# Kernel tuning notes

Measured on AMD Instinct MI355X. Metric: run time of the kernel, lower is better.

## Reference

```python
import jax, jax.numpy as jnp
import numpy as np


def setup_inputs() -> dict:
    key = jax.random.key(0)
    k1, k2 = jax.random.split(key)
    emb_in = jax.random.normal(k1, (2048, 32), dtype=jnp.float32)
    sum_weights = jax.random.normal(k2, (2048,), dtype=jnp.float32)
    return {"emb_in": emb_in, "sum_weights": sum_weights}


def reference(emb_in, sum_weights):
    # emb_in: [n, f], sum_weights: [n]
    n, f = emb_in.shape
    # a[k] = emb_in[k // n]  (each row repeated n times consecutively)
    a = jnp.repeat(emb_in, n, axis=0)          # [n*n, f]
    # b[k] = emb_in[k % n]   (whole tensor tiled n times)
    b = jnp.tile(emb_in, (n, 1))               # [n*n, f]
    # weights column matches b: w[k] = sum_weights[k % n]
    w = jnp.tile(sum_weights[:, None], (n, 1)) # [n*n, 1]
    sample = jnp.concatenate((a, b, w), axis=1)  # [n*n, 2*f + 1]
    return sample
```

## Files before the change

kernel.cpp:

```cpp
#include <hip/hip_runtime.h>


#define NROWS 2048u
#define BLOCK_ROWS 512u
#define WAVE_ROWS 128u
#define SLAB_ROWS 16u
#define NSLABS 8u
#define SLAB_FLOATS (SLAB_ROWS * 65u)
#define SLAB_F4 (SLAB_FLOATS / 4u)

typedef float f32x4 __attribute__((ext_vector_type(4)));

__global__ __launch_bounds__(256) void expand_pipe(
    const float* __restrict__ emb,
    const float* __restrict__ sw,
    f32x4* __restrict__ out)
{
    __shared__ __align__(16) float lds[4][2][SLAB_FLOATS];

    const unsigned tid  = threadIdx.x;
    const unsigned wave = tid >> 6;
    const unsigned lane = tid & 63u;

    const unsigned r0 = blockIdx.x * BLOCK_ROWS + wave * WAVE_ROWS;
    const unsigned i  = r0 >> 11;
    const unsigned j0 = r0 & (NROWS - 1u);

    const float vi = emb[i * 32u + (lane & 31u)];
    const unsigned rbase = (lane >> 5) * 8u;
#pragma unroll
    for (unsigned b = 0; b < 2u; ++b)
#pragma unroll
        for (unsigned rp = 0; rp < 8u; ++rp)
            lds[wave][b][(rbase + rp) * 65u + (lane & 31u)] = vi;

    const unsigned d0 = (lane >> 3) * 65u + 32u + (lane & 7u) * 4u;

    {
        const f32x4* ej = (const f32x4*)(emb + (size_t)j0 * 32u);
        const f32x4 pa = ej[lane];
        const f32x4 pb = ej[lane + 64u];
        const float ps = sw[j0 + (lane & 15u)];
        float* B = &lds[wave][0][0];
        B[d0 + 0u] = pa.x; B[d0 + 1u] = pa.y;
        B[d0 + 2u] = pa.z; B[d0 + 3u] = pa.w;
        B[d0 + 520u + 0u] = pb.x; B[d0 + 520u + 1u] = pb.y;
        B[d0 + 520u + 2u] = pb.z; B[d0 + 520u + 3u] = pb.w;
        if (lane < 16u) B[lane * 65u + 64u] = ps;
    }

#pragma unroll
    for (unsigned s = 0; s < NSLABS; ++s) {
        const unsigned cur = s & 1u;

        f32x4 pa, pb;
        float ps = 0.0f;
        if (s + 1u < NSLABS) {
            const f32x4* ej =
                (const f32x4*)(emb + (size_t)(j0 + (s + 1u) * SLAB_ROWS) * 32u);
            pa = ej[lane];
            pb = ej[lane + 64u];
            ps = sw[j0 + (s + 1u) * SLAB_ROWS + (lane & 15u)];
        }

        const f32x4* L4 = (const f32x4*)&lds[wave][cur][0];
        const unsigned obase = ((r0 + s * SLAB_ROWS) >> 4) * SLAB_F4;
#pragma unroll
        for (unsigned p = 0; p < 4u; ++p)
            out[obase + p * 64u + lane] = L4[p * 64u + lane];
        if (lane < 4u)
            out[obase + 256u + lane] = L4[256u + lane];

        if (s + 1u < NSLABS) {
            float* B = &lds[wave][cur ^ 1u][0];
            B[d0 + 0u] = pa.x; B[d0 + 1u] = pa.y;
            B[d0 + 2u] = pa.z; B[d0 + 3u] = pa.w;
            B[d0 + 520u + 0u] = pb.x; B[d0 + 520u + 1u] = pb.y;
            B[d0 + 520u + 2u] = pb.z; B[d0 + 520u + 3u] = pb.w;
            if (lane < 16u) B[lane * 65u + 64u] = ps;
        }
    }
}

extern "C" void kernel_launch(void* const* d_in, const int* in_sizes, int n_in,
                              void* d_out, int out_size, void* d_ws, size_t ws_size,
                              hipStream_t stream) {
    const float* emb = (const float*)d_in[0];
    const float* sw  = (const float*)d_in[1];
    f32x4* out       = (f32x4*)d_out;

    const unsigned blocks = (NROWS * NROWS) / BLOCK_ROWS;
    expand_pipe<<<dim3(blocks), dim3(256), 0, stream>>>(emb, sw, out);
}
```

Measured before the change: 203.9 us.

## Replace LDS double buffer with register double buffering and two-slab prefetch

Drops the per-wave second LDS buffer and instead reads each assembled slab from LDS into registers, alternating between two register sets. Global loads for the next slabs are issued two slabs ahead, and the LDS slot is rewritten right after being read, so stores to the output come straight from registers. The aim is to halve LDS use and hide global load latency behind the output stores, at the cost of higher VGPR pressure. The kernel is store-bound, so the gain may be small.

```diff
diff --git a/kernel.cpp b/kernel.cpp
--- a/kernel.cpp
+++ b/kernel.cpp
@@ -11,12 +11,12 @@
 
 typedef float f32x4 __attribute__((ext_vector_type(4)));
 
-__global__ __launch_bounds__(256) void expand_pipe(
+__global__ __launch_bounds__(256) void expand_rra(
     const float* __restrict__ emb,
     const float* __restrict__ sw,
     f32x4* __restrict__ out)
 {
-    __shared__ __align__(16) float lds[4][2][SLAB_FLOATS];
+    __shared__ __align__(16) float lds[4][SLAB_FLOATS];
 
     const unsigned tid  = threadIdx.x;
     const unsigned wave = tid >> 6;
@@ -26,60 +26,84 @@
     const unsigned i  = r0 >> 11;
     const unsigned j0 = r0 & (NROWS - 1u);
 
+    float* W = &lds[wave][0];
+    const f32x4* L4 = (const f32x4*)W;
+
     const float vi = emb[i * 32u + (lane & 31u)];
     const unsigned rbase = (lane >> 5) * 8u;
 #pragma unroll
-    for (unsigned b = 0; b < 2u; ++b)
-#pragma unroll
-        for (unsigned rp = 0; rp < 8u; ++rp)
-            lds[wave][b][(rbase + rp) * 65u + (lane & 31u)] = vi;
+    for (unsigned rp = 0; rp < 8u; ++rp)
+        W[(rbase + rp) * 65u + (lane & 31u)] = vi;
 
     const unsigned d0 = (lane >> 3) * 65u + 32u + (lane & 7u) * 4u;
 
+    f32x4 RA0, RA1, RA2, RA3, RA4;
+    f32x4 RB0, RB1, RB2, RB3, RB4;
+    f32x4 pA0, pA1, pB0, pB1;
+    float psA, psB;
+
     {
         const f32x4* ej = (const f32x4*)(emb + (size_t)j0 * 32u);
-        const f32x4 pa = ej[lane];
-        const f32x4 pb = ej[lane + 64u];
-        const float ps = sw[j0 + (lane & 15u)];
-        float* B = &lds[wave][0][0];
-        B[d0 + 0u] = pa.x; B[d0 + 1u] = pa.y;
-        B[d0 + 2u] = pa.z; B[d0 + 3u] = pa.w;
-        B[d0 + 520u + 0u] = pb.x; B[d0 + 520u + 1u] = pb.y;
-        B[d0 + 520u + 2u] = pb.z; B[d0 + 520u + 3u] = pb.w;
-        if (lane < 16u) B[lane * 65u + 64u] = ps;
+        const f32x4 a0 = ej[lane];
+        const f32x4 a1 = ej[lane + 64u];
+        const float s0 = sw[j0 + (lane & 15u)];
+        W[d0 + 0u] = a0.x; W[d0 + 1u] = a0.y;
+        W[d0 + 2u] = a0.z; W[d0 + 3u] = a0.w;
+        W[d0 + 520u] = a1.x; W[d0 + 521u] = a1.y;
+        W[d0 + 522u] = a1.z; W[d0 + 523u] = a1.w;
+        if (lane < 16u) W[lane * 65u + 64u] = s0;
+    }
+    {
+        const f32x4* ej = (const f32x4*)(emb + (size_t)(j0 + SLAB_ROWS) * 32u);
+        pB0 = ej[lane];
+        pB1 = ej[lane + 64u];
+        psB = sw[j0 + SLAB_ROWS + (lane & 15u)];
+    }
+    RA0 = L4[lane];         RA1 = L4[64u + lane];
+    RA2 = L4[128u + lane];  RA3 = L4[192u + lane];
+    RA4 = L4[256u + (lane & 3u)];
+
+    const unsigned base0 = (r0 >> 4) * SLAB_F4;
+
+#define STEP(S, RC0, RC1, RC2, RC3, RC4, RN0, RN1, RN2, RN3, RN4,          \
+             PC0, PC1, PSC, PN0, PN1, PSN)                                 \
+    {                                                                      \
+        if ((S) + 1u < NSLABS) {                                           \
+            W[d0 + 0u] = PC0.x; W[d0 + 1u] = PC0.y;                        \
+            W[d0 + 2u] = PC0.z; W[d0 + 3u] = PC0.w;                        \
+            W[d0 + 520u] = PC1.x; W[d0 + 521u] = PC1.y;                    \
+            W[d0 + 522u] = PC1.z; W[d0 + 523u] = PC1.w;                    \
+            if (lane < 16u) W[lane * 65u + 64u] = PSC;                     \
+            RN0 = L4[lane];         RN1 = L4[64u + lane];                  \
+            RN2 = L4[128u + lane];  RN3 = L4[192u + lane];                 \
+            RN4 = L4[256u + (lane & 3u)];                                  \
+        }                                                                  \
+        {                                                                  \
+            const unsigned ob = base0 + (S) * SLAB_F4;                     \
+            out[ob + lane]        = RC0;                                   \
+            out[ob + 64u + lane]  = RC1;                                   \
+            out[ob + 128u + lane] = RC2;                                   \
+            out[ob + 192u + lane] = RC3;                                   \
+            if (lane < 4u) out[ob + 256u + lane] = RC4;                    \
+        }                                                                  \
+        if ((S) + 2u < NSLABS) {                                           \
+            const f32x4* ej = (const f32x4*)                               \
+                (emb + (size_t)(j0 + ((S) + 2u) * SLAB_ROWS) * 32u);       \
+            PN0 = ej[lane];                                                \
+            PN1 = ej[lane + 64u];                                          \
+            PSN = sw[j0 + ((S) + 2u) * SLAB_ROWS + (lane & 15u)];          \
+        }                                                                  \
     }
 
-#pragma unroll
-    for (unsigned s = 0; s < NSLABS; ++s) {
-        const unsigned cur = s & 1u;
-
-        f32x4 pa, pb;
-        float ps = 0.0f;
-        if (s + 1u < NSLABS) {
-            const f32x4* ej =
-                (const f32x4*)(emb + (size_t)(j0 + (s + 1u) * SLAB_ROWS) * 32u);
-            pa = ej[lane];
-            pb = ej[lane + 64u];
-            ps = sw[j0 + (s + 1u) * SLAB_ROWS + (lane & 15u)];
-        }
-
-        const f32x4* L4 = (const f32x4*)&lds[wave][cur][0];
-        const unsigned obase = ((r0 + s * SLAB_ROWS) >> 4) * SLAB_F4;
-#pragma unroll
-        for (unsigned p = 0; p < 4u; ++p)
-            out[obase + p * 64u + lane] = L4[p * 64u + lane];
-        if (lane < 4u)
-            out[obase + 256u + lane] = L4[256u + lane];
-
-        if (s + 1u < NSLABS) {
-            float* B = &lds[wave][cur ^ 1u][0];
-            B[d0 + 0u] = pa.x; B[d0 + 1u] = pa.y;
-            B[d0 + 2u] = pa.z; B[d0 + 3u] = pa.w;
-            B[d0 + 520u + 0u] = pb.x; B[d0 + 520u + 1u] = pb.y;
-            B[d0 + 520u + 2u] = pb.z; B[d0 + 520u + 3u] = pb.w;
-            if (lane < 16u) B[lane * 65u + 64u] = ps;
-        }
-    }
+    STEP(0u, RA0,RA1,RA2,RA3,RA4, RB0,RB1,RB2,RB3,RB4, pB0,pB1,psB, pA0,pA1,psA)
+    STEP(1u, RB0,RB1,RB2,RB3,RB4, RA0,RA1,RA2,RA3,RA4, pA0,pA1,psA, pB0,pB1,psB)
+    STEP(2u, RA0,RA1,RA2,RA3,RA4, RB0,RB1,RB2,RB3,RB4, pB0,pB1,psB, pA0,pA1,psA)
+    STEP(3u, RB0,RB1,RB2,RB3,RB4, RA0,RA1,RA2,RA3,RA4, pA0,pA1,psA, pB0,pB1,psB)
+    STEP(4u, RA0,RA1,RA2,RA3,RA4, RB0,RB1,RB2,RB3,RB4, pB0,pB1,psB, pA0,pA1,psA)
+    STEP(5u, RB0,RB1,RB2,RB3,RB4, RA0,RA1,RA2,RA3,RA4, pA0,pA1,psA, pB0,pB1,psB)
+    STEP(6u, RA0,RA1,RA2,RA3,RA4, RB0,RB1,RB2,RB3,RB4, pB0,pB1,psB, pA0,pA1,psA)
+    STEP(7u, RB0,RB1,RB2,RB3,RB4, RA0,RA1,RA2,RA3,RA4, pA0,pA1,psA, pB0,pB1,psB)
+#undef STEP
 }
 
 extern "C" void kernel_launch(void* const* d_in, const int* in_sizes, int n_in,
@@ -90,5 +114,5 @@
     f32x4* out       = (f32x4*)d_out;
 
     const unsigned blocks = (NROWS * NROWS) / BLOCK_ROWS;
-    expand_pipe<<<dim3(blocks), dim3(256), 0, stream>>>(emb, sw, out);
+    expand_rra<<<dim3(blocks), dim3(256), 0, stream>>>(emb, sw, out);
 }
```

Measured after the change: 217.5 us. +6.6%, slower.
